# Kernel tuning notes

Measured on AMD Instinct MI355X. Metric: run time of the kernel, lower is better.

## Reference

```python
import jax, jax.numpy as jnp
import numpy as np
from math import sqrt

DIM = 256
HEADS = 4
GROUPS = min(DIM // 4, 32)  # = 32
EPS = 1e-6


def setup_inputs() -> dict:
    key = jax.random.key(0)
    ks = jax.random.split(key, 10)
    B, C, H, W = 16, DIM, 32, 32
    x = jax.random.normal(ks[0], (B, C, H, W), dtype=jnp.float32)
    s = 1.0 / sqrt(C)
    inp = {
        'x': x,
        'gn_scale': jnp.ones((C,), jnp.float32),
        'gn_bias': jnp.zeros((C,), jnp.float32),
        'Wq': jax.random.normal(ks[1], (C, C), jnp.float32) * s,
        'bq': jnp.zeros((C,), jnp.float32),
        'Wk': jax.random.normal(ks[2], (C, C), jnp.float32) * s,
        'bk': jnp.zeros((C,), jnp.float32),
        'Wv': jax.random.normal(ks[3], (C, C), jnp.float32) * s,
        'bv': jnp.zeros((C,), jnp.float32),
        'Wp': jax.random.normal(ks[4], (C, C), jnp.float32) * s,
        'bp': jnp.zeros((C,), jnp.float32),
    }
    return inp


def _group_norm(x, scale, bias):
    B, C, H, W = x.shape
    xg = x.reshape(B, GROUPS, C // GROUPS, H, W)
    mean = xg.mean(axis=(2, 3, 4), keepdims=True)
    var = xg.var(axis=(2, 3, 4), keepdims=True)
    xg = (xg - mean) * jax.lax.rsqrt(var + EPS)
    x = xg.reshape(B, C, H, W)
    return x * scale[None, :, None, None] + bias[None, :, None, None]


def _lin_ch(x, W, b):
    # 1x1 conv / linear over channel dim: (B,C,H,W) x (C,Cout) -> (B,Cout,H,W)
    return jnp.einsum('bchw,cd->bdhw', x, W) + b[None, :, None, None]


def reference(x, gn_scale, gn_bias, Wq, bq, Wk, bk, Wv, bv, Wp, bp):
    B, C, H, W = x.shape
    dh = C // HEADS
    _x = _group_norm(x, gn_scale, gn_bias)
    q = _lin_ch(_x, Wq, bq).reshape(B, HEADS, dh, H, W)
    k = _lin_ch(_x, Wk, bk).reshape(B, HEADS, dh, H, W)
    v = _lin_ch(_x, Wv, bv).reshape(B, HEADS, dh, H, W)
    scores = jnp.einsum('bhdxy,bhdij->bhxyij', q, k) / sqrt(C)
    scores = scores.reshape(B, HEADS, H, W, H * W)
    weights = jax.nn.softmax(scores, axis=-1).reshape(B, HEADS, H, W, H, W)
    h = jnp.einsum('bhxyij,bhdij->bhdxy', weights, v).reshape(B, C, H, W)
    h = _lin_ch(h, Wp, bp)
    ret = (x + h) / sqrt(2.0)
    return ret
```

## Files before the change

### kernel.cpp

```cpp
#include <hip/hip_runtime.h>
#include <hip/hip_bf16.h>

#define BATCH 16
#define CH    256
#define HW    1024
#define NH    4
#define DH    64
#define NG    32
#define CPG   8
#define EPSV  1e-6f

#define QSCALE 0.090168440055558706f

typedef __bf16 bf16x8 __attribute__((ext_vector_type(8)));
typedef float  f32x4  __attribute__((ext_vector_type(4)));

__device__ __forceinline__ unsigned short f2bf(float f) {
    union { __hip_bfloat16 h; unsigned short u; } cv;
    cv.h = __float2bfloat16(f);
    return cv.u;
}

__device__ __forceinline__ unsigned int fbits(float f) {
    union { float f; unsigned int u; } cv; cv.f = f; return cv.u;
}

__device__ __forceinline__ void gld_lds16(const unsigned short* g, unsigned short* l) {
    __builtin_amdgcn_global_load_lds(
        (const __attribute__((address_space(1))) void*)g,
        (__attribute__((address_space(3))) void*)l, 16, 0, 0);
}

__global__ void prep_kernel(const float* Wq, const float* Wk, const float* Wv,
                            const float* Wp, const float* bq, const float* bk,
                            const float* bv, unsigned short* wqkv_t,
                            unsigned short* wp_t, float* bqkv) {
    int idx = blockIdx.x * 256 + threadIdx.x;
    if (idx < 768 * 256) {
        int n = idx >> 8, c = idx & 255;
        const float* W = (n < 256) ? Wq : (n < 512) ? Wk : Wv;
        int d = n & 255;
        wqkv_t[idx] = f2bf(W[c * 256 + d]);
    } else if (idx < 768 * 256 + 256 * 256) {
        int j = idx - 768 * 256;
        int n = j >> 8, c = j & 255;
        wp_t[j] = f2bf(Wp[c * 256 + n]);
    }
    if (idx < 768)
        bqkv[idx] = (idx < 256) ? bq[idx] : (idx < 512) ? bk[idx - 256] : bv[idx - 512];
}

__global__ void gn_stats_kernel(const float* x, float* gmean, float* grstd) {
    int bg = blockIdx.x;
    const float* p = x + (size_t)bg * (CPG * HW);
    int t = threadIdx.x;
    float s = 0.f, ss = 0.f;
    for (int i = t; i < CPG * HW; i += 256) {
        float v = p[i];
        s += v; ss += v * v;
    }
    for (int o = 32; o; o >>= 1) { s += __shfl_down(s, o); ss += __shfl_down(ss, o); }
    __shared__ float as[4], ass[4];
    int w = t >> 6;
    if ((t & 63) == 0) { as[w] = s; ass[w] = ss; }
    __syncthreads();
    if (t == 0) {
        float S = as[0] + as[1] + as[2] + as[3];
        float SS = ass[0] + ass[1] + ass[2] + ass[3];
        float mean = S / (float)(CPG * HW);
        float var = SS / (float)(CPG * HW) - mean * mean;
        gmean[bg] = mean;
        grstd[bg] = rsqrtf(var + EPSV);
    }
}

__global__ void gn_apply_kernel(const float* x, const float* scale, const float* bias,
                                const float* gmean, const float* grstd,
                                unsigned short* xn_t) {
    int b = blockIdx.y;
    int p0 = blockIdx.x * 64;
    int t = threadIdx.x;
    __shared__ unsigned short lds[64][CH + 8];
    int pp = t & 63, cq = t >> 6;
    const float* xb = x + (size_t)b * CH * HW;
    for (int c0 = 0; c0 < CH; c0 += 4) {
        int c = c0 + cq;
        int g = b * NG + (c >> 3);
        float m = gmean[g], r = grstd[g];
        float v = xb[(size_t)c * HW + p0 + pp];
        lds[pp][c] = f2bf((v - m) * r * scale[c] + bias[c]);
    }
    __syncthreads();
    unsigned short* dst = xn_t + ((size_t)b * HW + p0) * CH;
    for (int pass = 0; pass < 4; pass++) {
        int row = pass * 16 + (t >> 4);
        int c = (t & 15) * 16;
        ulonglong2 v0 = *reinterpret_cast<ulonglong2*>(&lds[row][c]);
        ulonglong2 v1 = *reinterpret_cast<ulonglong2*>(&lds[row][c + 8]);
        *reinterpret_cast<ulonglong2*>(dst + (size_t)row * CH + c) = v0;
        *reinterpret_cast<ulonglong2*>(dst + (size_t)row * CH + c + 8) = v1;
    }
}

__global__ __launch_bounds__(256) void qkv_kernel(const unsigned short* xn_t,
        const unsigned short* wqkv_t, const float* bqkv,
        unsigned short* qb, unsigned short* kb, unsigned short* vb) {
    int t = threadIdx.x;
    int wv = t >> 6, lane = t & 63, quad = lane >> 4, ln = lane & 15;
    int wr = wv >> 1, wc = wv & 1;
    int m0 = blockIdx.x * 128 + wr * 64;
    int n0 = blockIdx.y * 128 + wc * 64;

    f32x4 acc[4][4] = {};
    for (int k0 = 0; k0 < CH; k0 += 32) {
        int koff = k0 + quad * 8;
        bf16x8 af[4], bfr[4];
#pragma unroll
        for (int i = 0; i < 4; i++)
            af[i] = *reinterpret_cast<const bf16x8*>(xn_t + (size_t)(m0 + i * 16 + ln) * CH + koff);
#pragma unroll
        for (int j = 0; j < 4; j++)
            bfr[j] = *reinterpret_cast<const bf16x8*>(wqkv_t + (size_t)(n0 + j * 16 + ln) * CH + koff);
#pragma unroll
        for (int i = 0; i < 4; i++)
#pragma unroll
            for (int j = 0; j < 4; j++)
                acc[i][j] = __builtin_amdgcn_mfma_f32_16x16x32_bf16(af[i], bfr[j], acc[i][j], 0, 0, 0);
    }
#pragma unroll
    for (int j = 0; j < 4; j++) {
        int n = n0 + j * 16 + ln;
        float bias = bqkv[n];
        int which = n >> 8;
        int dh_ = n & 255;
        int head = dh_ >> 6, d = dh_ & 63;
#pragma unroll
        for (int i = 0; i < 4; i++) {
            int mb = m0 + i * 16 + quad * 4;
            int bi = mb >> 10, p = mb & 1023;
            int bh = bi * NH + head;
            if (which < 2) {
                unsigned short* dst = (which == 0 ? qb : kb) + (size_t)bh * HW * DH;
                float sc = (which == 0) ? QSCALE : 1.0f;
#pragma unroll
                for (int r = 0; r < 4; r++)
                    dst[(size_t)(p + r) * DH + d] = f2bf((acc[i][j][r] + bias) * sc);
            } else {
                unsigned short* dst = vb + ((size_t)bh * DH + d) * HW + p;
                ushort4 pk4;
                pk4.x = f2bf(acc[i][j][0] + bias);
                pk4.y = f2bf(acc[i][j][1] + bias);
                pk4.z = f2bf(acc[i][j][2] + bias);
                pk4.w = f2bf(acc[i][j][3] + bias);
                *reinterpret_cast<ushort4*>(dst) = pk4;
            }
        }
    }
}

__global__ __launch_bounds__(256) void attn_kernel(const unsigned short* qb,
        const unsigned short* kb, const unsigned short* vb, unsigned short* h_t) {
    int qblk = blockIdx.x, bh = blockIdx.y;
    int t = threadIdx.x;
    int wv = t >> 6, lane = t & 63, quad = lane >> 4, ln = lane & 15;
    int q0 = qblk * 128 + wv * 32;

    const unsigned short* Q = qb + (size_t)bh * HW * DH;
    const unsigned short* K = kb + (size_t)bh * HW * DH;
    const unsigned short* V = vb + (size_t)bh * DH * HW;

    __shared__ __align__(16) unsigned short kbuf[2][4096];
    __shared__ __align__(16) unsigned short vbuf[2][4096];
    __shared__ __align__(16) unsigned short pbuf[4][2][16][72];

    int c_a = wv * 64 + lane;
    int c_b = 256 + wv * 64 + lane;
    int pa = c_a >> 3, ja = (c_a & 7) ^ (pa & 7);
    int pb = c_b >> 3, jb = (c_b & 7) ^ (pb & 7);
    const unsigned short* pka = K + (size_t)pa * DH + ja * 8;
    const unsigned short* pkb = K + (size_t)pb * DH + jb * 8;
    const unsigned short* pva = V + (size_t)pa * HW + ja * 8;
    const unsigned short* pvb = V + (size_t)pb * HW + jb * 8;
    int lofs_a = wv * 512, lofs_b = 2048 + wv * 512;

    int koffs[4][2];
#pragma unroll
    for (int mt = 0; mt < 4; mt++) {
        int p = mt * 16 + ln, sw = p & 7;
#pragma unroll
        for (int kk = 0; kk < 2; kk++)
            koffs[mt][kk] = p * 64 + (((kk * 4 + quad) ^ sw) * 8);
    }

    bf16x8 qf[2][2];
#pragma unroll
    for (int nq = 0; nq < 2; nq++)
#pragma unroll
        for (int kk = 0; kk < 2; kk++)
            qf[nq][kk] = *reinterpret_cast<const bf16x8*>(
                Q + (size_t)(q0 + nq * 16 + ln) * DH + kk * 32 + quad * 8);

    f32x4 ls[2] = {};
    f32x4 o[2][4] = {};

    gld_lds16(pka, &kbuf[0][lofs_a]);
    gld_lds16(pkb, &kbuf[0][lofs_b]);
    gld_lds16(pva, &vbuf[0][lofs_a]);
    gld_lds16(pvb, &vbuf[0][lofs_b]);
    pka += 64 * DH; pkb += 64 * DH; pva += 64; pvb += 64;

#define ATTN_TILE(B, DO_STAGE)                                                      \
    {                                                                               \
        __syncthreads();                                                            \
        if (DO_STAGE) {                                                             \
            gld_lds16(pka, &kbuf[B ^ 1][lofs_a]);                                   \
            gld_lds16(pkb, &kbuf[B ^ 1][lofs_b]);                                   \
            gld_lds16(pva, &vbuf[B ^ 1][lofs_a]);                                   \
            gld_lds16(pvb, &vbuf[B ^ 1][lofs_b]);                                   \
            pka += 64 * DH; pkb += 64 * DH; pva += 64; pvb += 64;                   \
        }                                                                           \
        bf16x8 kf[4][2], vf[4][2];                                                  \
        _Pragma("unroll")                                                           \
        for (int mt = 0; mt < 4; mt++) {                                            \
            _Pragma("unroll")                                                       \
            for (int kk = 0; kk < 2; kk++) {                                        \
                kf[mt][kk] = *reinterpret_cast<const bf16x8*>(&kbuf[B][koffs[mt][kk]]); \
                vf[mt][kk] = *reinterpret_cast<const bf16x8*>(&vbuf[B][koffs[mt][kk]]); \
            }                                                                       \
        }                                                                           \
        f32x4 s[2][4] = {};                                                         \
        _Pragma("unroll")                                                           \
        for (int nq = 0; nq < 2; nq++)                                              \
            _Pragma("unroll")                                                       \
            for (int mt = 0; mt < 4; mt++) {                                        \
                s[nq][mt] = __builtin_amdgcn_mfma_f32_16x16x32_bf16(kf[mt][0], qf[nq][0], s[nq][mt], 0, 0, 0); \
                s[nq][mt] = __builtin_amdgcn_mfma_f32_16x16x32_bf16(kf[mt][1], qf[nq][1], s[nq][mt], 0, 0, 0); \
            }                                                                       \
        _Pragma("unroll")                                                           \
        for (int nq = 0; nq < 2; nq++)                                              \
            _Pragma("unroll")                                                       \
            for (int mt = 0; mt < 4; mt++) {                                        \
                float e0 = __builtin_amdgcn_exp2f(s[nq][mt][0]);                    \
                float e1 = __builtin_amdgcn_exp2f(s[nq][mt][1]);                    \
                float e2 = __builtin_amdgcn_exp2f(s[nq][mt][2]);                    \
                float e3 = __builtin_amdgcn_exp2f(s[nq][mt][3]);                    \
                ls[nq][0] += e0; ls[nq][1] += e1;                                   \
                ls[nq][2] += e2; ls[nq][3] += e3;                                   \
                uint2 pk2;                                                          \
                pk2.x = __builtin_amdgcn_perm(fbits(e1), fbits(e0), 0x07060302u);   \
                pk2.y = __builtin_amdgcn_perm(fbits(e3), fbits(e2), 0x07060302u);   \
                *reinterpret_cast<uint2*>(&pbuf[wv][nq][ln][mt * 16 + quad * 4]) = pk2; \
            }                                                                       \
        _Pragma("unroll")                                                           \
        for (int nq = 0; nq < 2; nq++)                                              \
            _Pragma("unroll")                                                       \
            for (int kk = 0; kk < 2; kk++) {                                        \
                bf16x8 pf = *reinterpret_cast<const bf16x8*>(&pbuf[wv][nq][ln][kk * 32 + quad * 8]); \
                _Pragma("unroll")                                                   \
                for (int mt = 0; mt < 4; mt++)                                      \
                    o[nq][mt] = __builtin_amdgcn_mfma_f32_16x16x32_bf16(vf[mt][kk], pf, o[nq][mt], 0, 0, 0); \
            }                                                                       \
    }

    for (int u = 0; u < 8; u++) {
        ATTN_TILE(0, true)
        ATTN_TILE(1, (u < 7))
    }
#undef ATTN_TILE

    int b_ = bh >> 2, head = bh & 3;
#pragma unroll
    for (int nq = 0; nq < 2; nq++) {
        float lsum = ls[nq][0] + ls[nq][1] + ls[nq][2] + ls[nq][3];
        lsum += __shfl_xor(lsum, 16);
        lsum += __shfl_xor(lsum, 32);
        float inv = 1.0f / lsum;
        unsigned short* dst = h_t + ((size_t)b_ * HW + q0 + nq * 16 + ln) * CH + head * DH;
#pragma unroll
        for (int mt = 0; mt < 4; mt++) {
            ushort4 pk4;
            pk4.x = f2bf(o[nq][mt][0] * inv);
            pk4.y = f2bf(o[nq][mt][1] * inv);
            pk4.z = f2bf(o[nq][mt][2] * inv);
            pk4.w = f2bf(o[nq][mt][3] * inv);
            *reinterpret_cast<ushort4*>(dst + mt * 16 + quad * 4) = pk4;
        }
    }
}

__global__ __launch_bounds__(256) void proj_kernel(const unsigned short* h_t,
        const unsigned short* wp_t, const float* bp, const float* x, float* out) {
    int t = threadIdx.x;
    int wv = t >> 6, lane = t & 63, quad = lane >> 4, ln = lane & 15;
    int wr = wv >> 1, wc = wv & 1;
    int m0 = blockIdx.x * 128 + wr * 64;
    int n0 = blockIdx.y * 128 + wc * 64;

    f32x4 acc[4][4] = {};
    for (int k0 = 0; k0 < CH; k0 += 32) {
        int koff = k0 + quad * 8;
        bf16x8 af[4], bfr[4];
#pragma unroll
        for (int i = 0; i < 4; i++)
            af[i] = *reinterpret_cast<const bf16x8*>(h_t + (size_t)(m0 + i * 16 + ln) * CH + koff);
#pragma unroll
        for (int j = 0; j < 4; j++)
            bfr[j] = *reinterpret_cast<const bf16x8*>(wp_t + (size_t)(n0 + j * 16 + ln) * CH + koff);
#pragma unroll
        for (int i = 0; i < 4; i++)
#pragma unroll
            for (int j = 0; j < 4; j++)
                acc[i][j] = __builtin_amdgcn_mfma_f32_16x16x32_bf16(af[i], bfr[j], acc[i][j], 0, 0, 0);
    }
    const float inv_s2 = 0.70710678118654752440f;
#pragma unroll
    for (int j = 0; j < 4; j++) {
        int n = n0 + j * 16 + ln;
        float bias = bp[n];
#pragma unroll
        for (int i = 0; i < 4; i++) {
            int mb = m0 + i * 16 + quad * 4;
            int bi = mb >> 10, p = mb & 1023;
            size_t off = ((size_t)(bi * CH + n)) * HW + p;
            float4 xv = *reinterpret_cast<const float4*>(x + off);
            float4 ov;
            ov.x = (xv.x + acc[i][j][0] + bias) * inv_s2;
            ov.y = (xv.y + acc[i][j][1] + bias) * inv_s2;
            ov.z = (xv.z + acc[i][j][2] + bias) * inv_s2;
            ov.w = (xv.w + acc[i][j][3] + bias) * inv_s2;
            *reinterpret_cast<float4*>(out + off) = ov;
        }
    }
}

extern "C" void kernel_launch(void* const* d_in, const int* in_sizes, int n_in,
                              void* d_out, int out_size, void* d_ws, size_t ws_size,
                              hipStream_t stream) {
    const float* x        = (const float*)d_in[0];
    const float* gn_scale = (const float*)d_in[1];
    const float* gn_bias  = (const float*)d_in[2];
    const float* Wq = (const float*)d_in[3];
    const float* bq = (const float*)d_in[4];
    const float* Wk = (const float*)d_in[5];
    const float* bk = (const float*)d_in[6];
    const float* Wv = (const float*)d_in[7];
    const float* bv = (const float*)d_in[8];
    const float* Wp = (const float*)d_in[9];
    const float* bp = (const float*)d_in[10];
    float* out = (float*)d_out;

    char* ws = (char*)d_ws;
    float*          gmean  = (float*)(ws + 0);
    float*          grstd  = (float*)(ws + 2048);
    float*          bqkv   = (float*)(ws + 4096);
    unsigned short* wqkv_t = (unsigned short*)(ws + 8192);
    unsigned short* wp_t   = (unsigned short*)(ws + 401408);
    unsigned short* xn_t   = (unsigned short*)(ws + 532480);
    unsigned short* h_t    = xn_t;
    unsigned short* qb     = (unsigned short*)(ws + 8921088);
    unsigned short* kb     = (unsigned short*)(ws + 17309696);
    unsigned short* vb     = (unsigned short*)(ws + 25698304);

    prep_kernel<<<1024, 256, 0, stream>>>(Wq, Wk, Wv, Wp, bq, bk, bv, wqkv_t, wp_t, bqkv);
    gn_stats_kernel<<<512, 256, 0, stream>>>(x, gmean, grstd);
    gn_apply_kernel<<<dim3(16, 16), 256, 0, stream>>>(x, gn_scale, gn_bias, gmean, grstd, xn_t);
    qkv_kernel<<<dim3(128, 6), 256, 0, stream>>>(xn_t, wqkv_t, bqkv, qb, kb, vb);
    attn_kernel<<<dim3(8, 64), 256, 0, stream>>>(qb, kb, vb, h_t);
    proj_kernel<<<dim3(128, 2), 256, 0, stream>>>(h_t, wp_t, bp, x, out);
}
```

Before: 179.2 us.

## Fuse GroupNorm apply into QKV GEMM and shrink proj tiles

```diff
diff --git a/kernel.cpp b/kernel.cpp
--- a/kernel.cpp
+++ b/kernel.cpp
@@ -50,77 +50,92 @@
         bqkv[idx] = (idx < 256) ? bq[idx] : (idx < 512) ? bk[idx - 256] : bv[idx - 512];
 }
 
-__global__ void gn_stats_kernel(const float* x, float* gmean, float* grstd) {
+__global__ void gn_stats_kernel(const float* x, const float* scale, const float* bias,
+                                float* coefA, float* coefB) {
     int bg = blockIdx.x;
-    const float* p = x + (size_t)bg * (CPG * HW);
+    const float4* p = reinterpret_cast<const float4*>(x + (size_t)bg * (CPG * HW));
     int t = threadIdx.x;
     float s = 0.f, ss = 0.f;
-    for (int i = t; i < CPG * HW; i += 256) {
-        float v = p[i];
-        s += v; ss += v * v;
+    for (int i = t; i < CPG * HW / 4; i += 256) {
+        float4 v = p[i];
+        s += v.x + v.y + v.z + v.w;
+        ss += v.x * v.x + v.y * v.y + v.z * v.z + v.w * v.w;
     }
     for (int o = 32; o; o >>= 1) { s += __shfl_down(s, o); ss += __shfl_down(ss, o); }
     __shared__ float as[4], ass[4];
     int w = t >> 6;
     if ((t & 63) == 0) { as[w] = s; ass[w] = ss; }
     __syncthreads();
-    if (t == 0) {
+    if (t < 8) {
         float S = as[0] + as[1] + as[2] + as[3];
         float SS = ass[0] + ass[1] + ass[2] + ass[3];
         float mean = S / (float)(CPG * HW);
         float var = SS / (float)(CPG * HW) - mean * mean;
-        gmean[bg] = mean;
-        grstd[bg] = rsqrtf(var + EPSV);
-    }
-}
-
-__global__ void gn_apply_kernel(const float* x, const float* scale, const float* bias,
-                                const float* gmean, const float* grstd,
-                                unsigned short* xn_t) {
-    int b = blockIdx.y;
-    int p0 = blockIdx.x * 64;
-    int t = threadIdx.x;
-    __shared__ unsigned short lds[64][CH + 8];
-    int pp = t & 63, cq = t >> 6;
-    const float* xb = x + (size_t)b * CH * HW;
-    for (int c0 = 0; c0 < CH; c0 += 4) {
-        int c = c0 + cq;
-        int g = b * NG + (c >> 3);
-        float m = gmean[g], r = grstd[g];
-        float v = xb[(size_t)c * HW + p0 + pp];
-        lds[pp][c] = f2bf((v - m) * r * scale[c] + bias[c]);
-    }
-    __syncthreads();
-    unsigned short* dst = xn_t + ((size_t)b * HW + p0) * CH;
-    for (int pass = 0; pass < 4; pass++) {
-        int row = pass * 16 + (t >> 4);
-        int c = (t & 15) * 16;
-        ulonglong2 v0 = *reinterpret_cast<ulonglong2*>(&lds[row][c]);
-        ulonglong2 v1 = *reinterpret_cast<ulonglong2*>(&lds[row][c + 8]);
-        *reinterpret_cast<ulonglong2*>(dst + (size_t)row * CH + c) = v0;
-        *reinterpret_cast<ulonglong2*>(dst + (size_t)row * CH + c + 8) = v1;
-    }
-}
-
-__global__ __launch_bounds__(256) void qkv_kernel(const unsigned short* xn_t,
+        float rstd = rsqrtf(var + EPSV);
+        int b = bg >> 5, g = bg & 31;
+        int c = g * CPG + t;
+        float a = rstd * scale[c];
+        coefA[b * CH + c] = a;
+        coefB[b * CH + c] = bias[c] - mean * a;
+    }
+}
+
+__global__ __launch_bounds__(256) void qkv_kernel(const float* x,
+        const float* coefA, const float* coefB,
         const unsigned short* wqkv_t, const float* bqkv,
         unsigned short* qb, unsigned short* kb, unsigned short* vb) {
     int t = threadIdx.x;
     int wv = t >> 6, lane = t & 63, quad = lane >> 4, ln = lane & 15;
     int wr = wv >> 1, wc = wv & 1;
-    int m0 = blockIdx.x * 128 + wr * 64;
+    int bx = blockIdx.x;
+    int m0 = bx * 128 + wr * 64;
     int n0 = blockIdx.y * 128 + wc * 64;
+    int bb = bx >> 3;
+    int p0 = (bx & 7) * 128;
+
+    __shared__ __align__(16) unsigned short lds_a[128][40];
+
+    const float* xb = x + (size_t)bb * CH * HW + p0;
+    const float* cA = coefA + bb * CH;
+    const float* cB = coefB + bb * CH;
+
+    int sp = t & 127;
+    int sbase = (t >> 7) * 2;
 
     f32x4 acc[4][4] = {};
     for (int k0 = 0; k0 < CH; k0 += 32) {
-        int koff = k0 + quad * 8;
+        bf16x8 wpk[2];
+#pragma unroll
+        for (int rep = 0; rep < 2; rep++) {
+            int s = sbase + rep;
+            int cb = k0 + s * 8;
+            union { bf16x8 v8; __hip_bfloat162 h2[4]; } u;
+#pragma unroll
+            for (int j = 0; j < 4; j++) {
+                float v0 = fmaf(xb[(size_t)(cb + 2 * j)     * HW + sp], cA[cb + 2 * j],     cB[cb + 2 * j]);
+                float v1 = fmaf(xb[(size_t)(cb + 2 * j + 1) * HW + sp], cA[cb + 2 * j + 1], cB[cb + 2 * j + 1]);
+                u.h2[j] = __float22bfloat162_rn(float2{v0, v1});
+            }
+            wpk[rep] = u.v8;
+        }
+        __syncthreads();
+#pragma unroll
+        for (int rep = 0; rep < 2; rep++) {
+            int s = sbase + rep;
+            int phys = s ^ (sp & 3);
+            *reinterpret_cast<bf16x8*>(&lds_a[sp][phys * 8]) = wpk[rep];
+        }
+        __syncthreads();
         bf16x8 af[4], bfr[4];
 #pragma unroll
-        for (int i = 0; i < 4; i++)
-            af[i] = *reinterpret_cast<const bf16x8*>(xn_t + (size_t)(m0 + i * 16 + ln) * CH + koff);
+        for (int i = 0; i < 4; i++) {
+            int p = wr * 64 + i * 16 + ln;
+            af[i] = *reinterpret_cast<const bf16x8*>(&lds_a[p][(quad ^ (p & 3)) * 8]);
+        }
 #pragma unroll
         for (int j = 0; j < 4; j++)
-            bfr[j] = *reinterpret_cast<const bf16x8*>(wqkv_t + (size_t)(n0 + j * 16 + ln) * CH + koff);
+            bfr[j] = *reinterpret_cast<const bf16x8*>(
+                wqkv_t + (size_t)(n0 + j * 16 + ln) * CH + k0 + quad * 8);
 #pragma unroll
         for (int i = 0; i < 4; i++)
 #pragma unroll
@@ -293,21 +308,21 @@
     int t = threadIdx.x;
     int wv = t >> 6, lane = t & 63, quad = lane >> 4, ln = lane & 15;
     int wr = wv >> 1, wc = wv & 1;
-    int m0 = blockIdx.x * 128 + wr * 64;
+    int m0 = blockIdx.x * 64 + wr * 32;
     int n0 = blockIdx.y * 128 + wc * 64;
 
-    f32x4 acc[4][4] = {};
+    f32x4 acc[2][4] = {};
     for (int k0 = 0; k0 < CH; k0 += 32) {
         int koff = k0 + quad * 8;
-        bf16x8 af[4], bfr[4];
-#pragma unroll
-        for (int i = 0; i < 4; i++)
+        bf16x8 af[2], bfr[4];
+#pragma unroll
+        for (int i = 0; i < 2; i++)
             af[i] = *reinterpret_cast<const bf16x8*>(h_t + (size_t)(m0 + i * 16 + ln) * CH + koff);
 #pragma unroll
         for (int j = 0; j < 4; j++)
             bfr[j] = *reinterpret_cast<const bf16x8*>(wp_t + (size_t)(n0 + j * 16 + ln) * CH + koff);
 #pragma unroll
-        for (int i = 0; i < 4; i++)
+        for (int i = 0; i < 2; i++)
 #pragma unroll
             for (int j = 0; j < 4; j++)
                 acc[i][j] = __builtin_amdgcn_mfma_f32_16x16x32_bf16(af[i], bfr[j], acc[i][j], 0, 0, 0);
@@ -318,7 +333,7 @@
         int n = n0 + j * 16 + ln;
         float bias = bp[n];
 #pragma unroll
-        for (int i = 0; i < 4; i++) {
+        for (int i = 0; i < 2; i++) {
             int mb = m0 + i * 16 + quad * 4;
             int bi = mb >> 10, p = mb & 1023;
             size_t off = ((size_t)(bi * CH + n)) * HW + p;
@@ -350,21 +365,19 @@
     float* out = (float*)d_out;
 
     char* ws = (char*)d_ws;
-    float*          gmean  = (float*)(ws + 0);
-    float*          grstd  = (float*)(ws + 2048);
-    float*          bqkv   = (float*)(ws + 4096);
-    unsigned short* wqkv_t = (unsigned short*)(ws + 8192);
-    unsigned short* wp_t   = (unsigned short*)(ws + 401408);
-    unsigned short* xn_t   = (unsigned short*)(ws + 532480);
-    unsigned short* h_t    = xn_t;
-    unsigned short* qb     = (unsigned short*)(ws + 8921088);
-    unsigned short* kb     = (unsigned short*)(ws + 17309696);
-    unsigned short* vb     = (unsigned short*)(ws + 25698304);
+    float*          bqkv   = (float*)(ws + 0);
+    float*          coefA  = (float*)(ws + 4096);
+    float*          coefB  = (float*)(ws + 20480);
+    unsigned short* wqkv_t = (unsigned short*)(ws + 36864);
+    unsigned short* wp_t   = (unsigned short*)(ws + 430080);
+    unsigned short* h_t    = (unsigned short*)(ws + 1048576);
+    unsigned short* qb     = (unsigned short*)(ws + 9437184);
+    unsigned short* kb     = (unsigned short*)(ws + 17825792);
+    unsigned short* vb     = (unsigned short*)(ws + 26214400);
 
     prep_kernel<<<1024, 256, 0, stream>>>(Wq, Wk, Wv, Wp, bq, bk, bv, wqkv_t, wp_t, bqkv);
-    gn_stats_kernel<<<512, 256, 0, stream>>>(x, gmean, grstd);
-    gn_apply_kernel<<<dim3(16, 16), 256, 0, stream>>>(x, gn_scale, gn_bias, gmean, grstd, xn_t);
-    qkv_kernel<<<dim3(128, 6), 256, 0, stream>>>(xn_t, wqkv_t, bqkv, qb, kb, vb);
+    gn_stats_kernel<<<512, 256, 0, stream>>>(x, gn_scale, gn_bias, coefA, coefB);
+    qkv_kernel<<<dim3(128, 6), 256, 0, stream>>>(x, coefA, coefB, wqkv_t, bqkv, qb, kb, vb);
     attn_kernel<<<dim3(8, 64), 256, 0, stream>>>(qb, kb, vb, h_t);
-    proj_kernel<<<dim3(128, 2), 256, 0, stream>>>(h_t, wp_t, bp, x, out);
-}
+    proj_kernel<<<dim3(256, 2), 256, 0, stream>>>(h_t, wp_t, bp, x, out);
+}
```

Result: faster. 162.3 us (-9.4%).
